# Kernel tuning notes

Hardware: AMD Instinct MI355X
Metric: run time of the kernel (lower is better)

## Reference

```python
import jax, jax.numpy as jnp
from jax import lax
import numpy as np

NE = 8          # ne_num
IDX_REF = 4     # ne_num // 2
EPS_BN = 1e-5


def conv2d(x, w, b=None, pad=0):
    out = lax.conv_general_dilated(x, w, (1, 1), [(pad, pad), (pad, pad)],
                                   dimension_numbers=('NCHW', 'OIHW', 'NCHW'))
    if b is not None:
        out = out + b[None, :, None, None]
    return out


def bn(x, gamma, beta):
    # training-mode batch norm (biased variance), as nn.BatchNorm2d in train()
    mu = x.mean(axis=(0, 2, 3), keepdims=True)
    var = x.var(axis=(0, 2, 3), keepdims=True)
    xn = (x - mu) * lax.rsqrt(var + EPS_BN)
    return xn * gamma[None, :, None, None] + beta[None, :, None, None]


def gauss_win(sigma):
    # sigma: (B,1). window_size=3 -> bias = [-1, 0, -1]; pop center of 3x3 -> (B,8)
    bias = jnp.array([-1.0, 0.0, -1.0], dtype=sigma.dtype)
    g = jnp.exp(bias[None, :] / (2.0 * sigma ** 2))            # (B,3)
    w1 = g / g.sum(axis=1, keepdims=True)                      # (B,3)
    w2 = (w1[:, :, None] * w1[:, None, :]).reshape(-1, 9)      # (B,9)
    return jnp.concatenate([w2[:, :4], w2[:, 5:]], axis=1)     # (B,8) center removed


def bilinear(img, y, x):
    # img: (B,H,W); y,x: (B,K,H,W) float sample coords; zero padding outside
    B, H, W = img.shape
    y0 = jnp.floor(y); x0 = jnp.floor(x)
    wy1 = y - y0; wy0 = 1.0 - wy1
    wx1 = x - x0; wx0 = 1.0 - wx1
    imgf = img.reshape(B, -1)

    def gather(yi, xi):
        yii = yi.astype(jnp.int32); xii = xi.astype(jnp.int32)
        valid = (yii >= 0) & (yii < H) & (xii >= 0) & (xii < W)
        idx = jnp.clip(yii, 0, H - 1) * W + jnp.clip(xii, 0, W - 1)
        v = jnp.take_along_axis(imgf, idx.reshape(B, -1), axis=1).reshape(idx.shape)
        return jnp.where(valid, v, 0.0)

    return (wy0 * wx0 * gather(y0, x0) + wy0 * wx1 * gather(y0, x0 + 1.0)
            + wy1 * wx0 * gather(y0 + 1.0, x0) + wy1 * wx1 * gather(y0 + 1.0, x0 + 1.0))


def modulated_deform_conv_1x9(fusion, offset, mask):
    # ModulatedDeformConvFunction with weight=ones(1,1,3,3), bias=0, stride=1,
    # pad=1, dilation=1, groups=1, deformable_groups=1.
    # fusion: (B,1,H,W); offset: (B,9,2,H,W) [per-neighbor (dy,dx)]; mask: (B,9,H,W)
    B, _, H, W = fusion.shape
    k = jnp.arange(9)
    py = (k // 3 - 1).astype(fusion.dtype)[None, :, None, None]
    px = (k % 3 - 1).astype(fusion.dtype)[None, :, None, None]
    hh = jnp.arange(H, dtype=fusion.dtype)[None, None, :, None]
    ww = jnp.arange(W, dtype=fusion.dtype)[None, None, None, :]
    y = hh + py + offset[:, :, 0]
    x = ww + px + offset[:, :, 1]
    samp = bilinear(fusion[:, 0], y, x)            # (B,9,H,W)
    return (mask * samp).sum(axis=1, keepdims=True)  # (B,1,H,W)


def _forward(feat, g1_w, g1_g, g1_b, g2_w, g2_g, g2_b, g3_w, g3_bias,
             f1_w, f1_g, f1_b, f2_w, f2_bias,
             s1_w, s1_b, s2_w, s2_b, s3_w, s3_b,
             oa1_w, oa1_g, oa1_b, oa2_w, oa2_g, oa2_b, oa3_w, oa3_bias,
             aff_scale):
    B, _, H, W = feat.shape
    # guid branch (5x5 convs)
    guid = jax.nn.relu(bn(conv2d(feat, g1_w, pad=2), g1_g, g1_b))
    guid = jax.nn.relu(bn(conv2d(guid, g2_w, pad=2), g2_g, g2_b))
    guid = conv2d(guid, g3_w, g3_bias, pad=2)                      # (B,8,H,W)
    # fuse branch
    f = jax.nn.relu(bn(conv2d(feat, f1_w, pad=1), f1_g, f1_b))
    fusion = jnp.tanh(conv2d(f, f2_w, f2_bias, pad=1))             # (B,1,H,W)
    # sigma branch (CAM, detached input)
    fd = lax.stop_gradient(feat)
    p = fd.mean(axis=(2, 3))                                       # (B,32)
    h = jax.nn.celu(p @ s1_w.T + s1_b)
    h = jax.nn.celu(h @ s2_w.T + s2_b)
    sigma = jax.nn.relu(h @ s3_w.T + s3_b) + 0.001                 # (B,1)
    # get_off_aff(guid, sigma, sigma_gamma=0.2, window_size=3)
    oa = jax.nn.relu(bn(conv2d(guid, oa1_w, pad=2), oa1_g, oa1_b))
    oa = jax.nn.relu(bn(conv2d(oa, oa2_w, pad=2), oa2_g, oa2_b))
    oa = conv2d(oa, oa3_w, oa3_bias, pad=2)                        # (B,24,H,W)
    o1, o2, affc = jnp.split(oa, 3, axis=1)                        # each (B,8,H,W)
    off = jnp.concatenate([o1, o2], axis=1).reshape(B, NE, 2, H, W)
    zero_ref = jnp.zeros((B, 1, 2, H, W), dtype=off.dtype)
    offset = jnp.concatenate([off[:, :IDX_REF], zero_ref, off[:, IDX_REF:]], axis=1)  # (B,9,2,H,W)
    gk = gauss_win(sigma + 0.2)                                    # (B,8)
    aff = jnp.tanh(affc) / (aff_scale + 1e-5) + gk[:, :, None, None]
    sa = jnp.abs(aff).sum(axis=1, keepdims=True) + 1e-5
    sa = jnp.maximum(sa, 1.0)
    aff = aff / sa
    aff_ref = 1.0 - aff.sum(axis=1, keepdims=True)
    aff9 = jnp.concatenate([aff[:, :IDX_REF], aff_ref, aff[:, IDX_REF:]], axis=1)  # (B,9,H,W)
    # gauss_filter (times=1) + abs
    gfusion = jnp.abs(modulated_deform_conv_1x9(fusion, offset, aff9))
    return gfusion


def setup_inputs() -> dict:
    key = jax.random.key(0)
    ks = list(jax.random.split(key, 32))
    B, C, H, W = 8, 32, 320, 320
    ne = NE
    d = {}
    d['feat'] = jax.random.normal(ks[0], (B, C, H, W), jnp.float32)

    def wconv(k, o, i, s):
        return jax.random.normal(k, (o, i, s, s), jnp.float32) * (1.0 / np.sqrt(i * s * s))

    def wlin(k, o, i):
        return jax.random.normal(k, (o, i), jnp.float32) * (1.0 / np.sqrt(i))

    # guid: 32->32 (5), 32->8 (5), 8->8 (5, bias)
    d['g1_w'] = wconv(ks[1], C, C, 5); d['g1_g'] = jnp.ones(C) + 0.1 * jax.random.normal(ks[2], (C,)); d['g1_b'] = 0.1 * jax.random.normal(ks[3], (C,))
    d['g2_w'] = wconv(ks[4], ne, C, 5); d['g2_g'] = jnp.ones(ne) + 0.1 * jax.random.normal(ks[5], (ne,)); d['g2_b'] = 0.1 * jax.random.normal(ks[6], (ne,))
    d['g3_w'] = wconv(ks[7], ne, ne, 5); d['g3_bias'] = 0.1 * jax.random.normal(ks[8], (ne,))
    # fuse: 32->32 (3), 32->1 (3, bias)
    d['f1_w'] = wconv(ks[9], C, C, 3); d['f1_g'] = jnp.ones(C) + 0.1 * jax.random.normal(ks[10], (C,)); d['f1_b'] = 0.1 * jax.random.normal(ks[11], (C,))
    d['f2_w'] = wconv(ks[12], 1, C, 3); d['f2_bias'] = 0.1 * jax.random.normal(ks[13], (1,))
    # gen_sigma CAM: 32->16->16->1
    d['s1_w'] = wlin(ks[14], 16, C); d['s1_b'] = 0.1 * jax.random.normal(ks[15], (16,))
    d['s2_w'] = wlin(ks[16], 16, 16); d['s2_b'] = 0.1 * jax.random.normal(ks[17], (16,))
    d['s3_w'] = wlin(ks[18], 1, 16); d['s3_b'] = 0.1 * jax.random.normal(ks[19], (1,))
    # conv_off_aff: 8->8 (5), 8->24 (5), 24->24 (5, bias)
    d['oa1_w'] = wconv(ks[20], ne, ne, 5); d['oa1_g'] = jnp.ones(ne) + 0.1 * jax.random.normal(ks[21], (ne,)); d['oa1_b'] = 0.1 * jax.random.normal(ks[22], (ne,))
    d['oa2_w'] = wconv(ks[23], 3 * ne, ne, 5); d['oa2_g'] = jnp.ones(3 * ne) + 0.1 * jax.random.normal(ks[24], (3 * ne,)); d['oa2_b'] = 0.1 * jax.random.normal(ks[25], (3 * ne,))
    d['oa3_w'] = wconv(ks[26], 3 * ne, 3 * ne, 5); d['oa3_bias'] = 0.1 * jax.random.normal(ks[27], (3 * ne,))
    # aff_scale_const = aff_gamma * ne_num = 0.5 * 8
    d['aff_scale'] = jnp.full((1,), 4.0, jnp.float32)
    return d


def reference(feat, g1_w, g1_g, g1_b, g2_w, g2_g, g2_b, g3_w, g3_bias,
              f1_w, f1_g, f1_b, f2_w, f2_bias,
              s1_w, s1_b, s2_w, s2_b, s3_w, s3_b,
              oa1_w, oa1_g, oa1_b, oa2_w, oa2_g, oa2_b, oa3_w, oa3_bias,
              aff_scale):
    return _forward(feat, g1_w, g1_g, g1_b, g2_w, g2_g, g2_b, g3_w, g3_bias,
                    f1_w, f1_g, f1_b, f2_w, f2_bias,
                    s1_w, s1_b, s2_w, s2_b, s3_w, s3_b,
                    oa1_w, oa1_g, oa1_b, oa2_w, oa2_g, oa2_b, oa3_w, oa3_bias,
                    aff_scale)
```

## Files before the change

### kernel.cpp

```cpp
#include <hip/hip_runtime.h>
#include <hip/hip_bf16.h>
#include <math.h>

#define B_   8
#define H_   320
#define W_   320
#define HW_  (320*320)

typedef __attribute__((ext_vector_type(8))) short bf16x8;
typedef __attribute__((ext_vector_type(4))) short bf16x4s;
typedef __attribute__((ext_vector_type(4))) float f32x4;

__device__ __forceinline__ short f2b(float v){
    __hip_bfloat16 h = __float2bfloat16(v);
    return *(short*)&h;
}
__device__ __forceinline__ float bf2f(short v){
    unsigned u = ((unsigned)(unsigned short)v) << 16;
    return __uint_as_float(u);
}

__global__ void convert_k(const float* __restrict__ in, short* __restrict__ out,
                          float* __restrict__ psum){
    const int b  = blockIdx.y;
    const int px = blockIdx.x*256 + threadIdx.x;
    const float* src = in + (long)b*32*HW_ + px;
    short* dst = out + ((long)b*HW_ + px)*32;
    float f[32];
    short v[32];
    #pragma unroll
    for (int c=0;c<32;++c){ f[c] = src[(long)c*HW_]; v[c] = f2b(f[c]); }
    #pragma unroll
    for (int s=0;s<4;++s)
        *(bf16x8*)(dst + s*8) = *(bf16x8*)(v + s*8);
    #pragma unroll
    for (int c=0;c<32;++c){
        float s = f[c];
        #pragma unroll
        for (int o=1;o<64;o<<=1) s += __shfl_xor(s, o, 64);
        f[c] = s;
    }
    __shared__ float red[4][32];
    const int lane = threadIdx.x & 63, wid = threadIdx.x >> 6;
    if (lane < 32) red[wid][lane] = f[lane];
    __syncthreads();
    if (threadIdx.x < 32)
        atomicAdd(&psum[b*32 + threadIdx.x],
                  red[0][threadIdx.x]+red[1][threadIdx.x]+red[2][threadIdx.x]+red[3][threadIdx.x]);
}

__global__ void repack_k(const float* __restrict__ sf1, const float* __restrict__ sf2,
                         const float* __restrict__ sg1, const float* __restrict__ sg2,
                         const float* __restrict__ sg3, const float* __restrict__ so1,
                         const float* __restrict__ so2, const float* __restrict__ so3,
                         short* __restrict__ dst){
    const int cum[8]  = {9216,13824,39424,52224,55808,59392,66560,92160};
    const int CINs[8] = {32,32,32,32, 8, 8, 8,24};
    const int CIps[8] = {32,32,32,32, 8, 8, 8,32};
    const int COUTs[8]= {32, 1,32, 8, 8, 8,24,24};
    const int MTs[8]  = { 2, 1, 2, 1, 1, 1, 2, 2};
    const int Ks[8]   = { 3, 3, 5, 5, 5, 5, 5, 5};
    int i = blockIdx.x*256 + threadIdx.x;
    if (i >= 92160) return;
    int s = 0;
    while (i >= cum[s]) ++s;
    const int base = s ? cum[s-1] : 0;
    const int il = i - base;
    const float* src = (s==0)?sf1:(s==1)?sf2:(s==2)?sg1:(s==3)?sg2:(s==4)?sg3:(s==5)?so1:(s==6)?so2:so3;
    const int kl   = il & 31;
    const int co_l = (il >> 5) & 15;
    const int rem  = il >> 9;
    const int MT = MTs[s];
    const int mt = rem % MT;
    const int c  = rem / MT;
    const int K = Ks[s];
    int tap, ci;
    if (CIps[s] == 32){ tap = (c % K)*K + (c / K); ci = kl; }
    else              { tap = c*4 + (kl>>3); ci = kl & 7; }
    const int co = mt*16 + co_l;
    float v = 0.f;
    if (co < COUTs[s] && ci < CINs[s] && tap < K*K){
        const int ky = tap / K, kx = tap - ky*K;
        v = src[((co*CINs[s] + ci)*K + ky)*K + kx];
    }
    dst[i] = f2b(v);
}

__device__ __forceinline__
float deform_px(const float* val, const float* __restrict__ fus_b,
                const float* __restrict__ gk_b, float inv_s, int y, int x){
    float aff[8]; float sa = 0.f;
    #pragma unroll
    for (int n=0;n<8;++n){
        float a = tanhf(val[16+n]) * inv_s + gk_b[n];
        aff[n] = a; sa += fabsf(a);
    }
    sa += 1e-5f;
    sa = fmaxf(sa, 1.f);
    const float isa = 1.f/sa;
    float ssum = 0.f;
    #pragma unroll
    for (int n=0;n<8;++n){ aff[n] *= isa; ssum += aff[n]; }
    const float aff_ref = 1.f - ssum;

    float o = 0.f;
    #pragma unroll
    for (int k=0;k<9;++k){
        float dy, dx, m;
        if (k == 4){ dy = 0.f; dx = 0.f; m = aff_ref; }
        else {
            const int n = (k < 4) ? k : k-1;
            dy = val[2*n];
            dx = val[2*n+1];
            m  = aff[n];
        }
        float yy = (float)(y + k/3 - 1) + dy;
        float xx = (float)(x + k%3 - 1) + dx;
        float y0f = floorf(yy), x0f = floorf(xx);
        int   y0 = (int)y0f,    x0i = (int)x0f;
        float wy1 = yy - y0f, wy0 = 1.f - wy1;
        float wx1 = xx - x0f, wx0 = 1.f - wx1;
        float v00 = (y0  >=0 && y0  <H_ && x0i  >=0 && x0i  <W_) ? fus_b[ y0   *W_ + x0i  ] : 0.f;
        float v01 = (y0  >=0 && y0  <H_ && x0i+1>=0 && x0i+1<W_) ? fus_b[ y0   *W_ + x0i+1] : 0.f;
        float v10 = (y0+1>=0 && y0+1<H_ && x0i  >=0 && x0i  <W_) ? fus_b[(y0+1)*W_ + x0i  ] : 0.f;
        float v11 = (y0+1>=0 && y0+1<H_ && x0i+1>=0 && x0i+1<W_) ? fus_b[(y0+1)*W_ + x0i+1] : 0.f;
        o += m * (wy0*(wx0*v00 + wx1*v01) + wy1*(wx0*v10 + wx1*v11));
    }
    return fabsf(o);
}

template<int CIN, int CIp, int COUT, int MT, int K,
         bool IN_BN, bool OUT_STATS, int OUT_MODE, int OCP>
__global__ __launch_bounds__(256, 4)
void mconv_k(const void* __restrict__ inv,
             const float* __restrict__ bn_sum, const float* __restrict__ bn_sq,
             const float* __restrict__ gamma, const float* __restrict__ beta,
             const short* __restrict__ wr, const float* __restrict__ bias,
             void* __restrict__ outv,
             float* __restrict__ osum, float* __restrict__ osq,
             const float* __restrict__ fus, const float* __restrict__ gk,
             const float* __restrict__ aff_scale){
    constexpr int PAD = K/2;
    constexpr int TH  = 8;
    constexpr int LW  = 32 + K - 1;
    constexpr int LH  = TH + K - 1;
    constexpr int STR = (CIp==32) ? 40 : 8;
    constexpr int NTAPS  = K*K;
    constexpr int NCHUNK = (CIp==32) ? NTAPS : (NTAPS*CIp + 31)/32;
    constexpr int INB  = LH*LW*STR*2;
    constexpr int DUMPB = 256*33*4;
    constexpr int LDSB = (OUT_MODE==3 && INB < DUMPB) ? DUMPB : INB;

    __shared__ __align__(16) char ldsraw[LDSB];
    short* lds_in = (short*)ldsraw;
    __shared__ float sc_sh[2][32];
    __shared__ float red[2][4][32];

    const int tid = threadIdx.x;
    const int b   = blockIdx.z;
    const int x0  = blockIdx.x*32, y0 = blockIdx.y*TH;

    const int lane = tid & 63;
    const int wv   = tid >> 6;
    const int pxn  = lane & 15;
    const int quad = lane >> 4;
    const int row0 = 2*wv;

    if (IN_BN){
        if (tid < 32){
            float s = 1.f, sh2 = 0.f;
            if (tid < CIN){
                const float invN = 1.f/(float)(B_*HW_);
                float mu  = bn_sum[tid]*invN;
                float var = bn_sq[tid]*invN - mu*mu;
                s   = gamma[tid] * rsqrtf(var + 1e-5f);
                sh2 = beta[tid] - mu*s;
            }
            sc_sh[0][tid] = s;
            sc_sh[1][tid] = sh2;
        }
        __syncthreads();
    }

    constexpr int KC = (CIp==32) ? K : 1;
    bf16x8 aC[KC][MT];
    bf16x8 aAll[(CIp==8)?NCHUNK:1][MT];

    if constexpr (CIp == 32){
        #pragma unroll
        for (int ky=0; ky<K; ++ky)
            #pragma unroll
            for (int m=0;m<MT;++m)
                aC[ky][m] = *(const bf16x8*)(wr + ((ky*MT + m)*16 + pxn)*32 + quad*8);
    } else {
        #pragma unroll
        for (int c=0;c<NCHUNK;++c)
            #pragma unroll
            for (int m=0;m<MT;++m)
                aAll[c][m] = *(const bf16x8*)(wr + (((c*MT + m)*16 + pxn)*32 + quad*8));
    }

    {
        const short* src = (const short*)inv + (long)b*HW_*CIp;
        constexpr int SEGS = CIp/8;
        constexpr int NU = LH*LW*SEGS;
        constexpr int NIT = (NU + 255)/256;
        bf16x8 vv[NIT];
        int    la[NIT];
        bool   ib[NIT];
        #pragma unroll
        for (int it=0; it<NIT; ++it){
            const int u = tid + it*256;
            bf16x8 v = {0,0,0,0,0,0,0,0};
            bool inb = false;
            int addr = 0;
            if (u < NU){
                const int r   = u / (LW*SEGS);
                const int rem = u - r*(LW*SEGS);
                const int xl  = rem / SEGS;
                const int seg = rem - xl*SEGS;
                const int gy = y0 + r - PAD, gx = x0 + xl - PAD;
                addr = (r*LW + xl)*STR + seg*8;
                inb = (gy>=0 && gy<H_ && gx>=0 && gx<W_);
                if (inb)
                    v = *(const bf16x8*)(src + ((long)gy*W_ + gx)*CIp + seg*8);
            }
            vv[it] = v; la[it] = addr; ib[it] = inb;
        }
        __builtin_amdgcn_sched_barrier(0);
        #pragma unroll
        for (int it=0; it<NIT; ++it){
            const int u = tid + it*256;
            if (u < NU){
                bf16x8 v = vv[it];
                if (IN_BN && ib[it]){
                    const int seg = (u - (u/SEGS)*SEGS);
                    #pragma unroll
                    for (int j=0;j<8;++j){
                        float f = bf2f(v[j]);
                        f = fmaxf(fmaf(f, sc_sh[0][seg*8+j], sc_sh[1][seg*8+j]), 0.f);
                        v[j] = f2b(f);
                    }
                }
                *(bf16x8*)&lds_in[la[it]] = v;
            }
        }
    }
    __syncthreads();

    const f32x4 zero = {0.f, 0.f, 0.f, 0.f};
    f32x4 acc[2][MT][2];
    #pragma unroll
    for (int rr=0;rr<2;++rr)
        #pragma unroll
        for (int m=0;m<MT;++m){ acc[rr][m][0] = zero; acc[rr][m][1] = zero; }

    if constexpr (CIp == 32){
        const short* bbase = lds_in + (row0*LW + pxn)*STR + quad*8;
        #pragma unroll
        for (int kx=0; kx<K; ++kx){
            if (kx > 0){
                #pragma unroll
                for (int ky=0; ky<K; ++ky)
                    #pragma unroll
                    for (int m=0;m<MT;++m)
                        aC[ky][m] = *(const bf16x8*)(wr + (((kx*K+ky)*MT + m)*16 + pxn)*32 + quad*8);
            }
            bf16x8 bw[3][2];
            #pragma unroll
            for (int r=0;r<2;++r)
                #pragma unroll
                for (int n=0;n<2;++n)
                    bw[r][n] = *(const bf16x8*)(bbase + (r*LW + kx + n*16)*STR);
            __builtin_amdgcn_sched_barrier(0);
            #pragma unroll
            for (int ky=0; ky<K; ++ky){
                if (ky < K-1){
                    #pragma unroll
                    for (int n=0;n<2;++n)
                        bw[(ky+2)%3][n] = *(const bf16x8*)(bbase + ((ky+2)*LW + kx + n*16)*STR);
                }
                __builtin_amdgcn_sched_barrier(0);
                #pragma unroll
                for (int m=0;m<MT;++m){
                    acc[0][m][0] = __builtin_amdgcn_mfma_f32_16x16x32_bf16(aC[ky][m], bw[ky%3][0],     acc[0][m][0], 0,0,0);
                    acc[0][m][1] = __builtin_amdgcn_mfma_f32_16x16x32_bf16(aC[ky][m], bw[ky%3][1],     acc[0][m][1], 0,0,0);
                    acc[1][m][0] = __builtin_amdgcn_mfma_f32_16x16x32_bf16(aC[ky][m], bw[(ky+1)%3][0], acc[1][m][0], 0,0,0);
                    acc[1][m][1] = __builtin_amdgcn_mfma_f32_16x16x32_bf16(aC[ky][m], bw[(ky+1)%3][1], acc[1][m][1], 0,0,0);
                }
            }
        }
    } else {
        auto bptr = [&](int c, int rr)->const short*{
            const int row = row0 + rr;
            int t = c*4 + quad;
            if (t >= NTAPS) t = 0;
            const int ky = t / K, kx = t - ky*K;
            return lds_in + ((row+ky)*LW + kx + pxn)*STR;
        };

        bf16x8 bcp[2][2][2];
        #pragma unroll
        for (int rr=0;rr<2;++rr){
            const short* bp = bptr(0, rr);
            bcp[0][rr][0] = *(const bf16x8*)bp;
            bcp[0][rr][1] = *(const bf16x8*)(bp + 16*STR);
        }

        #pragma unroll
        for (int c=0; c<NCHUNK; ++c){
            if (c+1 < NCHUNK){
                #pragma unroll
                for (int rr=0;rr<2;++rr){
                    const short* bpn = bptr(c+1, rr);
                    bcp[(c+1)&1][rr][0] = *(const bf16x8*)bpn;
                    bcp[(c+1)&1][rr][1] = *(const bf16x8*)(bpn + 16*STR);
                }
            }
            __builtin_amdgcn_sched_barrier(0);
            #pragma unroll
            for (int m=0;m<MT;++m)
                #pragma unroll
                for (int rr=0;rr<2;++rr){
                    acc[rr][m][0] = __builtin_amdgcn_mfma_f32_16x16x32_bf16(aAll[c][m], bcp[c&1][rr][0], acc[rr][m][0], 0,0,0);
                    acc[rr][m][1] = __builtin_amdgcn_mfma_f32_16x16x32_bf16(aAll[c][m], bcp[c&1][rr][1], acc[rr][m][1], 0,0,0);
                }
        }
    }

    if (OUT_STATS){
        #pragma unroll
        for (int m=0;m<MT;++m){
            #pragma unroll
            for (int r=0;r<4;++r){
                float v  = acc[0][m][0][r] + acc[0][m][1][r]
                         + acc[1][m][0][r] + acc[1][m][1][r];
                float v2 = acc[0][m][0][r]*acc[0][m][0][r] + acc[0][m][1][r]*acc[0][m][1][r]
                         + acc[1][m][0][r]*acc[1][m][0][r] + acc[1][m][1][r]*acc[1][m][1][r];
                #pragma unroll
                for (int o=1;o<16;o<<=1){
                    v  += __shfl_xor(v,  o, 64);
                    v2 += __shfl_xor(v2, o, 64);
                }
                if (pxn == 0){
                    red[0][wv][m*16 + quad*4 + r] = v;
                    red[1][wv][m*16 + quad*4 + r] = v2;
                }
            }
        }
        __syncthreads();
        if (tid < MT*16 && tid < COUT){
            atomicAdd(&osum[tid], red[0][0][tid]+red[0][1][tid]+red[0][2][tid]+red[0][3][tid]);
            atomicAdd(&osq[tid],  red[1][0][tid]+red[1][1][tid]+red[1][2][tid]+red[1][3][tid]);
        }
    }

    if (OUT_MODE == 3){
        float* out = (float*)outv;
        __syncthreads();
        float* dumpf = (float*)ldsraw;
        #pragma unroll
        for (int rr=0;rr<2;++rr){
            const int row = row0 + rr;
            #pragma unroll
            for (int m=0;m<MT;++m)
                #pragma unroll
                for (int n=0;n<2;++n)
                    #pragma unroll
                    for (int r=0;r<4;++r)
                        dumpf[(row*32 + n*16 + pxn)*33 + (m*16 + quad*4 + r)] = acc[rr][m][n][r];
        }
        __syncthreads();
        {
            float val[24];
            #pragma unroll
            for (int c2=0;c2<24;++c2) val[c2] = dumpf[tid*33 + c2] + bias[c2];
            const int yy = y0 + (tid>>5), xx = x0 + (tid&31);
            const float inv_s = 1.f/(aff_scale[0] + 1e-5f);
            out[(long)b*HW_ + yy*W_ + xx] =
                deform_px(val, fus + (long)b*HW_, gk + b*8, inv_s, yy, xx);
        }
    } else if (OUT_MODE == 2){
        float* out = (float*)outv;
        #pragma unroll
        for (int rr=0;rr<2;++rr){
            const int y = y0 + row0 + rr;
            #pragma unroll
            for (int m=0;m<MT;++m){
                #pragma unroll
                for (int r=0;r<4;++r){
                    const int co = m*16 + quad*4 + r;
                    if (co < COUT){
                        float* op = out + (((long)b*COUT + co)*H_ + y)*W_ + x0;
                        #pragma unroll
                        for (int n=0;n<2;++n)
                            op[n*16 + pxn] = tanhf(acc[rr][m][n][r] + bias[co]);
                    }
                }
            }
        }
    } else {
        short* o = (short*)outv;
        #pragma unroll
        for (int rr=0;rr<2;++rr){
            const int y = y0 + row0 + rr;
            #pragma unroll
            for (int m=0;m<MT;++m){
                const int co0 = m*16 + quad*4;
                if (co0 < OCP){
                    #pragma unroll
                    for (int n=0;n<2;++n){
                        bf16x4s pk;
                        #pragma unroll
                        for (int r=0;r<4;++r){
                            float f = acc[rr][m][n][r];
                            if (OUT_MODE == 1) f += bias[co0+r];
                            pk[r] = f2b(f);
                        }
                        const long px = ((long)b*H_ + y)*W_ + x0 + n*16 + pxn;
                        *(bf16x4s*)(o + px*OCP + co0) = pk;
                    }
                }
            }
        }
    }
}

__global__ void sigma_k(const float* __restrict__ p,
                        const float* s1w, const float* s1b,
                        const float* s2w, const float* s2b,
                        const float* s3w, const float* s3b,
                        float* __restrict__ gk){
    const int b = threadIdx.x;
    if (b >= B_) return;
    float pb[32];
    for (int j=0;j<32;++j) pb[j] = p[b*32+j] * (1.f/(float)HW_);
    float h1[16], h2[16];
    for (int i=0;i<16;++i){
        float t = s1b[i];
        for (int j=0;j<32;++j) t = fmaf(pb[j], s1w[i*32+j], t);
        h1[i] = t > 0.f ? t : expm1f(t);
    }
    for (int i=0;i<16;++i){
        float t = s2b[i];
        for (int j=0;j<16;++j) t = fmaf(h1[j], s2w[i*16+j], t);
        h2[i] = t > 0.f ? t : expm1f(t);
    }
    float t = s3b[0];
    for (int j=0;j<16;++j) t = fmaf(h2[j], s3w[j], t);
    float sigma = fmaxf(t, 0.f) + 0.001f;
    float sg = sigma + 0.2f;
    float e = expf(-1.f/(2.f*sg*sg));
    float inv = 1.f/(2.f*e + 1.f);
    float a = e*inv, c = inv;
    float* g = gk + b*8;
    g[0]=a*a; g[1]=a*c; g[2]=a*a; g[3]=c*a; g[4]=c*a; g[5]=a*a; g[6]=a*c; g[7]=a*a;
}

extern "C" void kernel_launch(void* const* d_in, const int* in_sizes, int n_in,
                              void* d_out, int out_size, void* d_ws, size_t ws_size,
                              hipStream_t stream){
    const float* feat    = (const float*)d_in[0];
    const float* g1_w    = (const float*)d_in[1];
    const float* g1_g    = (const float*)d_in[2];
    const float* g1_b    = (const float*)d_in[3];
    const float* g2_w    = (const float*)d_in[4];
    const float* g2_g    = (const float*)d_in[5];
    const float* g2_b    = (const float*)d_in[6];
    const float* g3_w    = (const float*)d_in[7];
    const float* g3_bias = (const float*)d_in[8];
    const float* f1_w    = (const float*)d_in[9];
    const float* f1_g    = (const float*)d_in[10];
    const float* f1_b    = (const float*)d_in[11];
    const float* f2_w    = (const float*)d_in[12];
    const float* f2_bias = (const float*)d_in[13];
    const float* s1w     = (const float*)d_in[14];
    const float* s1b     = (const float*)d_in[15];
    const float* s2w     = (const float*)d_in[16];
    const float* s2b     = (const float*)d_in[17];
    const float* s3w     = (const float*)d_in[18];
    const float* s3b     = (const float*)d_in[19];
    const float* oa1_w   = (const float*)d_in[20];
    const float* oa1_g   = (const float*)d_in[21];
    const float* oa1_b   = (const float*)d_in[22];
    const float* oa2_w   = (const float*)d_in[23];
    const float* oa2_g   = (const float*)d_in[24];
    const float* oa2_b   = (const float*)d_in[25];
    const float* oa3_w   = (const float*)d_in[26];
    const float* oa3_bias= (const float*)d_in[27];
    const float* aff_scale=(const float*)d_in[28];
    float* out = (float*)d_out;

    char* ws = (char*)d_ws;
    short* FEAT = (short*)(ws + 0L);
    short* A1   = (short*)(ws + 52428800L);
    short* A2   = (short*)(ws + 104857600L);
    short* GUID = (short*)(ws + 117964800L);
    float* FUS  = (float*)(ws + 131072000L);
    float* SM   = (float*)(ws + 134348800L);
    short* OA2  = A1;

    float* sum = SM;
    float* sq  = SM + 320;
    float* p   = SM + 640;
    float* gk  = SM + 896;
    short* WBs = (short*)(SM + 960);
    short* w_f1 = WBs + 0;
    short* w_f2 = WBs + 9216;
    short* w_g1 = WBs + 13824;
    short* w_g2 = WBs + 39424;
    short* w_g3 = WBs + 52224;
    short* w_o1 = WBs + 55808;
    short* w_o2 = WBs + 59392;
    short* w_o3 = WBs + 66560;

    hipMemsetAsync(sum, 0, 896*sizeof(float), stream);

    repack_k<<<dim3(360), dim3(256), 0, stream>>>(
        f1_w, f2_w, g1_w, g2_w, g3_w, oa1_w, oa2_w, oa3_w, WBs);
    convert_k<<<dim3(HW_/256, B_), dim3(256), 0, stream>>>(feat, FEAT, p);

    sigma_k<<<dim3(1), dim3(64), 0, stream>>>(p, s1w, s1b, s2w, s2b, s3w, s3b, gk);

    const dim3 cgrid(10, 40, 8), cblk(256);
    #define MCONV(CIN,CIp,COUT,MT,K,IBN,OST,OM,OCP) \
        mconv_k<CIN,CIp,COUT,MT,K,IBN,OST,OM,OCP><<<cgrid,cblk,0,stream>>>

    MCONV(32,32,32,2,3,false,true ,0,32)(FEAT, nullptr, nullptr, nullptr, nullptr,
        w_f1, nullptr, A1, sum+0*64, sq+0*64, nullptr, nullptr, nullptr);
    MCONV(32,32, 1,1,3,true ,false,2, 0)(A1, sum+0*64, sq+0*64, f1_g, f1_b,
        w_f2, f2_bias, FUS, nullptr, nullptr, nullptr, nullptr, nullptr);

    MCONV(32,32,32,2,5,false,true ,0,32)(FEAT, nullptr, nullptr, nullptr, nullptr,
        w_g1, nullptr, A1, sum+1*64, sq+1*64, nullptr, nullptr, nullptr);
    MCONV(32,32, 8,1,5,true ,true ,0, 8)(A1, sum+1*64, sq+1*64, g1_g, g1_b,
        w_g2, nullptr, A2, sum+2*64, sq+2*64, nullptr, nullptr, nullptr);
    MCONV( 8, 8, 8,1,5,true ,false,1, 8)(A2, sum+2*64, sq+2*64, g2_g, g2_b,
        w_g3, g3_bias, GUID, nullptr, nullptr, nullptr, nullptr, nullptr);

    MCONV( 8, 8, 8,1,5,false,true ,0, 8)(GUID, nullptr, nullptr, nullptr, nullptr,
        w_o1, nullptr, A2, sum+3*64, sq+3*64, nullptr, nullptr, nullptr);
    MCONV( 8, 8,24,2,5,true ,true ,0,32)(A2, sum+3*64, sq+3*64, oa1_g, oa1_b,
        w_o2, nullptr, OA2, sum+4*64, sq+4*64, nullptr, nullptr, nullptr);
    MCONV(24,32,24,2,5,true ,false,3, 0)(OA2, sum+4*64, sq+4*64, oa2_g, oa2_b,
        w_o3, oa3_bias, out, nullptr, nullptr, FUS, gk, aff_scale);
    #undef MCONV
}
```

Before: 613.5 us.

## Store conv input tile as per-segment LDS planes and interleave weight reloads

The shared-memory input tile for 32-channel convs moves from a padded pixel-major layout (stride 40 shorts) to four channel-segment planes of 8 shorts per pixel. This shrinks LDS use and changes the bank access pattern of the B-operand reads. Weight fragments for the next kx column are now reloaded right after each ky's MFMAs instead of in one batch at the start of each kx, to overlap global loads with compute. The output dump buffer shrinks from a 33-float to a 25-float row stride and skips channels past 24, cutting LDS size. Each change may alter bank conflicts and register pressure.

```diff
diff --git a/kernel.cpp b/kernel.cpp
--- a/kernel.cpp
+++ b/kernel.cpp
@@ -144,11 +144,12 @@
     constexpr int TH  = 8;
     constexpr int LW  = 32 + K - 1;
     constexpr int LH  = TH + K - 1;
-    constexpr int STR = (CIp==32) ? 40 : 8;
+    constexpr int SEGS = CIp/8;
+    constexpr int PLANE = LH*LW*8 + 8;
     constexpr int NTAPS  = K*K;
     constexpr int NCHUNK = (CIp==32) ? NTAPS : (NTAPS*CIp + 31)/32;
-    constexpr int INB  = LH*LW*STR*2;
-    constexpr int DUMPB = 256*33*4;
+    constexpr int INB  = (CIp==32) ? (SEGS*PLANE*2) : (LH*LW*8*2);
+    constexpr int DUMPB = 256*25*4;
     constexpr int LDSB = (OUT_MODE==3 && INB < DUMPB) ? DUMPB : INB;
 
     __shared__ __align__(16) char ldsraw[LDSB];
@@ -202,7 +203,6 @@
 
     {
         const short* src = (const short*)inv + (long)b*HW_*CIp;
-        constexpr int SEGS = CIp/8;
         constexpr int NU = LH*LW*SEGS;
         constexpr int NIT = (NU + 255)/256;
         bf16x8 vv[NIT];
@@ -220,7 +220,7 @@
                 const int xl  = rem / SEGS;
                 const int seg = rem - xl*SEGS;
                 const int gy = y0 + r - PAD, gx = x0 + xl - PAD;
-                addr = (r*LW + xl)*STR + seg*8;
+                addr = seg*PLANE + (r*LW + xl)*8;
                 inb = (gy>=0 && gy<H_ && gx>=0 && gx<W_);
                 if (inb)
                     v = *(const bf16x8*)(src + ((long)gy*W_ + gx)*CIp + seg*8);
@@ -234,7 +234,7 @@
             if (u < NU){
                 bf16x8 v = vv[it];
                 if (IN_BN && ib[it]){
-                    const int seg = (u - (u/SEGS)*SEGS);
+                    const int seg = u - (u/SEGS)*SEGS;
                     #pragma unroll
                     for (int j=0;j<8;++j){
                         float f = bf2f(v[j]);
@@ -256,29 +256,22 @@
         for (int m=0;m<MT;++m){ acc[rr][m][0] = zero; acc[rr][m][1] = zero; }
 
     if constexpr (CIp == 32){
-        const short* bbase = lds_in + (row0*LW + pxn)*STR + quad*8;
+        const short* bbase = lds_in + quad*PLANE + (row0*LW + pxn)*8;
         #pragma unroll
         for (int kx=0; kx<K; ++kx){
-            if (kx > 0){
-                #pragma unroll
-                for (int ky=0; ky<K; ++ky)
-                    #pragma unroll
-                    for (int m=0;m<MT;++m)
-                        aC[ky][m] = *(const bf16x8*)(wr + (((kx*K+ky)*MT + m)*16 + pxn)*32 + quad*8);
-            }
             bf16x8 bw[3][2];
             #pragma unroll
             for (int r=0;r<2;++r)
                 #pragma unroll
                 for (int n=0;n<2;++n)
-                    bw[r][n] = *(const bf16x8*)(bbase + (r*LW + kx + n*16)*STR);
+                    bw[r][n] = *(const bf16x8*)(bbase + (r*LW + kx + n*16)*8);
             __builtin_amdgcn_sched_barrier(0);
             #pragma unroll
             for (int ky=0; ky<K; ++ky){
                 if (ky < K-1){
                     #pragma unroll
                     for (int n=0;n<2;++n)
-                        bw[(ky+2)%3][n] = *(const bf16x8*)(bbase + ((ky+2)*LW + kx + n*16)*STR);
+                        bw[(ky+2)%3][n] = *(const bf16x8*)(bbase + ((ky+2)*LW + kx + n*16)*8);
                 }
                 __builtin_amdgcn_sched_barrier(0);
                 #pragma unroll
@@ -288,6 +281,11 @@
                     acc[1][m][0] = __builtin_amdgcn_mfma_f32_16x16x32_bf16(aC[ky][m], bw[(ky+1)%3][0], acc[1][m][0], 0,0,0);
                     acc[1][m][1] = __builtin_amdgcn_mfma_f32_16x16x32_bf16(aC[ky][m], bw[(ky+1)%3][1], acc[1][m][1], 0,0,0);
                 }
+                if (kx+1 < K){
+                    #pragma unroll
+                    for (int m=0;m<MT;++m)
+                        aC[ky][m] = *(const bf16x8*)(wr + ((((kx+1)*K+ky)*MT + m)*16 + pxn)*32 + quad*8);
+                }
             }
         }
     } else {
@@ -296,7 +294,7 @@
             int t = c*4 + quad;
             if (t >= NTAPS) t = 0;
             const int ky = t / K, kx = t - ky*K;
-            return lds_in + ((row+ky)*LW + kx + pxn)*STR;
+            return lds_in + ((row+ky)*LW + kx + pxn)*8;
         };
 
         bf16x8 bcp[2][2][2];
@@ -304,7 +302,7 @@
         for (int rr=0;rr<2;++rr){
             const short* bp = bptr(0, rr);
             bcp[0][rr][0] = *(const bf16x8*)bp;
-            bcp[0][rr][1] = *(const bf16x8*)(bp + 16*STR);
+            bcp[0][rr][1] = *(const bf16x8*)(bp + 16*8);
         }
 
         #pragma unroll
@@ -314,7 +312,7 @@
                 for (int rr=0;rr<2;++rr){
                     const short* bpn = bptr(c+1, rr);
                     bcp[(c+1)&1][rr][0] = *(const bf16x8*)bpn;
-                    bcp[(c+1)&1][rr][1] = *(const bf16x8*)(bpn + 16*STR);
+                    bcp[(c+1)&1][rr][1] = *(const bf16x8*)(bpn + 16*8);
                 }
             }
             __builtin_amdgcn_sched_barrier(0);
@@ -363,18 +361,21 @@
         for (int rr=0;rr<2;++rr){
             const int row = row0 + rr;
             #pragma unroll
-            for (int m=0;m<MT;++m)
-                #pragma unroll
-                for (int n=0;n<2;++n)
+            for (int m=0;m<MT;++m){
+                if (m*16 + quad*4 < 24){
                     #pragma unroll
-                    for (int r=0;r<4;++r)
-                        dumpf[(row*32 + n*16 + pxn)*33 + (m*16 + quad*4 + r)] = acc[rr][m][n][r];
+                    for (int n=0;n<2;++n)
+                        #pragma unroll
+                        for (int r=0;r<4;++r)
+                            dumpf[(row*32 + n*16 + pxn)*25 + (m*16 + quad*4 + r)] = acc[rr][m][n][r];
+                }
+            }
         }
         __syncthreads();
         {
             float val[24];
             #pragma unroll
-            for (int c2=0;c2<24;++c2) val[c2] = dumpf[tid*33 + c2] + bias[c2];
+            for (int c2=0;c2<24;++c2) val[c2] = dumpf[tid*25 + c2] + bias[c2];
             const int yy = y0 + (tid>>5), xx = x0 + (tid&31);
             const float inv_s = 1.f/(aff_scale[0] + 1e-5f);
             out[(long)b*HW_ + yy*W_ + xx] =
```

New measurement: 596.8 us. 1.03x faster.
